# Performance work log

Hardware: AMD Instinct MI355X
Metric: run time of the kernel (lower is better)

## Reference

```python
import jax, jax.numpy as jnp
import numpy as np

B, N, L = 1, 256, 512
D_MSA, D_PAIR, H, D = 256, 128, 8, 32
SCALING = 1.0 / float(np.sqrt(D))
EPS = 1e-5


def layer_norm(x, g, b):
    mu = jnp.mean(x, axis=-1, keepdims=True)
    var = jnp.mean(jnp.square(x - mu), axis=-1, keepdims=True)
    return (x - mu) * jax.lax.rsqrt(var + EPS) * g + b


def setup_inputs() -> dict:
    key = jax.random.key(0)
    ks = jax.random.split(key, 16)
    inp = {
        "msa": jax.random.normal(ks[0], (B, N, L, D_MSA), dtype=jnp.float32),
        "pair": jax.random.normal(ks[1], (B, L, L, D_PAIR), dtype=jnp.float32),
        "ln_msa_g": 1.0 + 0.1 * jax.random.normal(ks[2], (D_MSA,), dtype=jnp.float32),
        "ln_msa_b": 0.1 * jax.random.normal(ks[3], (D_MSA,), dtype=jnp.float32),
        "ln_pair_g": 1.0 + 0.1 * jax.random.normal(ks[4], (D_PAIR,), dtype=jnp.float32),
        "ln_pair_b": 0.1 * jax.random.normal(ks[5], (D_PAIR,), dtype=jnp.float32),
        "w_q": 0.02 * jax.random.normal(ks[6], (D_MSA, H * D), dtype=jnp.float32),
        "w_k": 0.02 * jax.random.normal(ks[7], (D_MSA, H * D), dtype=jnp.float32),
        "w_v": 0.02 * jax.random.normal(ks[8], (D_MSA, H * D), dtype=jnp.float32),
        "w_b": 0.02 * jax.random.normal(ks[9], (D_PAIR, H), dtype=jnp.float32),
        "w_g": 0.02 * jax.random.normal(ks[10], (D_MSA, H * D), dtype=jnp.float32),
        "b_g": jnp.ones((H * D,), dtype=jnp.float32),
        "w_out": 0.02 * jax.random.normal(ks[11], (H * D, D_MSA), dtype=jnp.float32),
        "b_out": jnp.zeros((D_MSA,), dtype=jnp.float32),
        "mask": jax.random.randint(ks[12], (B, L), 0, 2, dtype=jnp.int32),
    }
    return inp


def reference(msa, pair, ln_msa_g, ln_msa_b, ln_pair_g, ln_pair_b,
              w_q, w_k, w_v, w_b, w_g, b_g, w_out, b_out, mask):
    # mask == 0 means padded/invalid position (torch: mask = mask == 0)
    pad = (mask == 0)  # [B, L] bool
    msa = jnp.nan_to_num(msa)
    pair = jnp.nan_to_num(pair)
    msa_n = layer_norm(msa, ln_msa_g, ln_msa_b)          # [B,N,L,d_msa]
    pair_n = layer_norm(pair, ln_pair_g, ln_pair_b)       # [B,L,L,d_pair]

    q = (msa_n @ w_q).reshape(B, N, L, H, D)
    k = (msa_n @ w_k).reshape(B, N, L, H, D)
    v = (msa_n @ w_v).reshape(B, N, L, H, D)
    bias = pair_n @ w_b                                    # [B,L,L,H]
    gate = jax.nn.sigmoid(msa_n @ w_g + b_g)               # [B,N,L,H*D]

    fill = pad[:, None, :, None, None]                     # [B,1,L,1,1]
    zero = jnp.zeros((), dtype=q.dtype)
    q = jnp.where(fill, zero, q)
    v = jnp.where(fill, zero, v)
    k = jnp.where(fill, zero, k) * jnp.asarray(SCALING, dtype=k.dtype)

    # reduce over both MSA-sequence dim n and head dim d
    attn = jnp.einsum('bnqhd,bnkhd->bqkh', q, k) + bias    # [B,L,L,H]
    mask2d = pad[:, :, None] | pad[:, None, :]             # [B,L,L]
    attn = jnp.where(mask2d[..., None], jnp.asarray(-1e9, attn.dtype), attn)
    attn = jax.nn.softmax(attn, axis=2)                    # softmax over k

    out = jnp.einsum('bqkh,bnkhd->bnqhd', attn, v).reshape(B, N, L, H * D)
    out = gate * out
    out = out @ w_out + b_out                              # [B,N,L,d_msa]
    out = jnp.where(pad[:, None, :, None], jnp.zeros((), out.dtype), out)
    return out
```

## Files before the change

kernel.cpp:

```cpp
#include <hip/hip_runtime.h>
#include <hip/hip_bf16.h>
#include <math.h>

typedef __bf16 bf16_t;
typedef float f32x4 __attribute__((ext_vector_type(4)));
typedef __bf16 bf16x8 __attribute__((ext_vector_type(8)));
typedef __bf16 bf16x4 __attribute__((ext_vector_type(4)));
typedef int i32x4 __attribute__((ext_vector_type(4)));

#define SCALING 0.17677669529663687f
#define LNEPS 1e-5f

#define OFF_QKG   0u
#define OFF_LOG   201326592u
#define OFF_BIAS  209715200u
#define OFF_P     218103808u
#define OFF_WT    222298112u
#define OFF_WTO   222822400u
#define OFF_FLAG  222953472u

#define GLOBAL_AS __attribute__((address_space(1)))
#define LDS_AS    __attribute__((address_space(3)))

static __device__ __forceinline__ f32x4 mfma16(bf16x8 a, bf16x8 b, f32x4 c) {
  return __builtin_amdgcn_mfma_f32_16x16x32_bf16(a, b, c, 0, 0, 0);
}

static __device__ __forceinline__ float ldf(const void* p, int i, int is32) {
  return is32 ? ((const float*)p)[i] : (float)((const bf16_t*)p)[i];
}
static __device__ __forceinline__ float scrubf(float x) {
  if (x != x) return 0.f;
  return fminf(fmaxf(x, -3.3e38f), 3.3e38f);
}

__global__ __launch_bounds__(256) void k_detect(const unsigned short* raw, int* flag) {
  __shared__ int s;
  int t = threadIdx.x;
  if (t == 0) s = 0;
  __syncthreads();
  int local = 0;
  for (int i = 0; i < 16; i++) {
    unsigned short u = raw[t * 16 + i];
    int e = (u >> 7) & 0xFF;
    if (e >= 170) local = 1;
  }
  if (local) s = 1;
  __syncthreads();
  if (t == 0) *flag = s;
}

__global__ __launch_bounds__(256) void k_transpose(
    const void* wq, const void* wk, const void* wv, const void* wg,
    const void* wout, const int* flag, bf16_t* wt_cat, bf16_t* wt_out) {
  int is32 = *flag;
  int idx = blockIdx.x * 256 + threadIdx.x;
  if (idx < 1024 * 256) {
    int c = idx >> 8, k = idx & 255;
    const void* src = (c < 256) ? wq : (c < 512) ? wk : (c < 768) ? wv : wg;
    wt_cat[c * 256 + (k ^ ((c & 7) << 3))] = (bf16_t)ldf(src, k * 256 + (c & 255), is32);
  } else {
    int i2 = idx - 1024 * 256;
    int c = i2 >> 8, k = i2 & 255;
    wt_out[c * 256 + k] = (bf16_t)ldf(wout, k * 256 + c, is32);
  }
}

__global__ __launch_bounds__(256) void k_ln(
    const void* msa, const void* g, const void* b, const int* flag,
    char* msaln, char* qkg_bytes) {
  int is32 = *flag;
  int t = threadIdx.x, lane = t & 63, w = t >> 6;
  int c0 = lane * 4;
  float gv[4], bv[4];
#pragma unroll
  for (int e = 0; e < 4; e++) { gv[e] = ldf(g, c0 + e, is32); bv[e] = ldf(b, c0 + e, is32); }
  int row0 = blockIdx.x * 64 + w * 16;
  for (int rr = 0; rr < 16; rr++) {
    int r = row0 + rr;
    float x[4];
    if (is32) {
      f32x4 v = *(const f32x4*)((const float*)msa + (size_t)r * 256 + c0);
#pragma unroll
      for (int e = 0; e < 4; e++) x[e] = scrubf(v[e]);
    } else {
      bf16x4 v = *(const bf16x4*)((const bf16_t*)msa + (size_t)r * 256 + c0);
#pragma unroll
      for (int e = 0; e < 4; e++) x[e] = scrubf((float)v[e]);
    }
    float s = x[0] + x[1] + x[2] + x[3];
    float sq = x[0] * x[0] + x[1] * x[1] + x[2] * x[2] + x[3] * x[3];
#pragma unroll
    for (int o = 32; o >= 1; o >>= 1) {
      s += __shfl_xor(s, o, 64);
      sq += __shfl_xor(sq, o, 64);
    }
    float mu = s * (1.f / 256.f);
    float var = sq * (1.f / 256.f) - mu * mu;
    float rs = rsqrtf(fmaxf(var, 0.f) + LNEPS);
    bf16x4 y;
#pragma unroll
    for (int e = 0; e < 4; e++) y[e] = (bf16_t)((x[e] - mu) * rs * gv[e] + bv[e]);
    int pc = (lane >> 1) ^ (r & 7);
    char* dst = is32 ? (msaln + (size_t)r * 512)
                     : (qkg_bytes + (size_t)r * 1536 + 512);
    *(bf16x4*)(dst + pc * 16 + (lane & 1) * 8) = y;
  }
}

__global__ __launch_bounds__(256) void k_pair_bias(
    const void* pair, const void* g, const void* b,
    const void* wb, const int* flag, float* bias_ws) {
  __shared__ float wbs[128 * 8];
  __shared__ float gs[128], bs[128];
  int is32 = *flag;
  int t = threadIdx.x;
  if (t < 128) { gs[t] = ldf(g, t, is32); bs[t] = ldf(b, t, is32); }
  for (int i = t; i < 1024; i += 256) wbs[i] = ldf(wb, i, is32);
  __syncthreads();
  int lane = t & 63, w = t >> 6;
  int j = lane & 7;
  int rowg = lane >> 3;
  float gr[16], br[16];
#pragma unroll
  for (int e = 0; e < 16; e++) { gr[e] = gs[j * 16 + e]; br[e] = bs[j * 16 + e]; }
  int row0 = blockIdx.x * 64 + w * 16;
#pragma unroll
  for (int pass = 0; pass < 2; pass++) {
    int row = row0 + pass * 8 + rowg;
    float x[16];
    if (is32) {
#pragma unroll
      for (int i = 0; i < 4; i++) {
        f32x4 v = *(const f32x4*)((const float*)pair + (size_t)row * 128 + j * 16 + i * 4);
#pragma unroll
        for (int e = 0; e < 4; e++) x[i * 4 + e] = scrubf(v[e]);
      }
    } else {
#pragma unroll
      for (int i = 0; i < 2; i++) {
        i32x4 raw = *(const i32x4*)((const bf16_t*)pair + (size_t)row * 128 + j * 16 + i * 8);
        const bf16_t* sp = (const bf16_t*)&raw;
#pragma unroll
        for (int e = 0; e < 8; e++) x[i * 8 + e] = scrubf((float)sp[e]);
      }
    }
    float s = 0.f, sq = 0.f;
#pragma unroll
    for (int e = 0; e < 16; e++) { s += x[e]; sq += x[e] * x[e]; }
#pragma unroll
    for (int o = 1; o <= 4; o <<= 1) {
      s += __shfl_xor(s, o, 64);
      sq += __shfl_xor(sq, o, 64);
    }
    float mu = s * (1.f / 128.f);
    float var = sq * (1.f / 128.f) - mu * mu;
    float rs = rsqrtf(fmaxf(var, 0.f) + LNEPS);
    float ph[8] = {0.f, 0.f, 0.f, 0.f, 0.f, 0.f, 0.f, 0.f};
#pragma unroll
    for (int e = 0; e < 16; e++) {
      float xn = (x[e] - mu) * rs * gr[e] + br[e];
      const float* wp = wbs + (j * 16 + e) * 8;
      f32x4 w0 = *(const f32x4*)wp;
      f32x4 w1 = *(const f32x4*)(wp + 4);
#pragma unroll
      for (int hh = 0; hh < 4; hh++) { ph[hh] += xn * w0[hh]; ph[4 + hh] += xn * w1[hh]; }
    }
#pragma unroll
    for (int o = 1; o <= 4; o <<= 1) {
#pragma unroll
      for (int hh = 0; hh < 8; hh++) ph[hh] += __shfl_xor(ph[hh], o, 64);
    }
    if (j == 0) {
      int qp = row >> 9, kp = row & 511;
      float* bp = bias_ws + (size_t)qp * 512 + kp;
#pragma unroll
      for (int hh = 0; hh < 8; hh++) bp[(size_t)hh * 262144] = ph[hh];
    }
  }
}

static __device__ __forceinline__ void issue_b(const bf16_t* wtc, int col0, int half,
                                               char* dst, int t) {
#pragma unroll
  for (int j = 0; j < 8; ++j) {
    int o = t * 16 + j * 4096;
    int row = o >> 8, within = o & 255;
    const char* src = (const char*)wtc + (size_t)(col0 + row) * 512 + half * 256 + within;
    __builtin_amdgcn_global_load_lds((const GLOBAL_AS void*)src,
                                     (LDS_AS void*)(dst + o), 16, 0, 0);
  }
}

__global__ __launch_bounds__(256, 2) void k_proj(
    const bf16_t* wt_cat, const void* bg, const int* mask, const int* flag,
    const char* msaln, bf16_t* qkg, bf16_t* vt) {
  __shared__ __align__(16) char lds[65536];
  char* B0 = lds + 32768;
  char* B1 = lds;
  int is32 = *flag;
  int t = threadIdx.x, lane = t & 63, wc = t >> 6;
  int hi = lane >> 4, cl = lane & 15;
  int row0 = blockIdx.x * 64;
  int rbase = row0 + hi * 4;

  unsigned padbits = 0;
#pragma unroll
  for (int m = 0; m < 4; ++m)
#pragma unroll
    for (int i = 0; i < 4; ++i)
      if (mask[(rbase + m * 16 + i) & 511] == 0) padbits |= 1u << (m * 4 + i);
  float bgv[2][2];
#pragma unroll
  for (int bb = 0; bb < 2; ++bb)
#pragma unroll
    for (int n = 0; n < 2; ++n)
      bgv[bb][n] = ldf(bg, bb * 128 + wc * 32 + n * 16 + cl, is32);

  {
    const char* abase = is32 ? msaln : ((const char*)qkg + 512);
    size_t astride = is32 ? 512 : 1536;
#pragma unroll
    for (int j = 0; j < 8; ++j) {
      int o = t * 16 + j * 4096;
      int row = o >> 9, within = o & 511;
      const char* src = abase + (size_t)(row0 + row) * astride + within;
      __builtin_amdgcn_global_load_lds((const GLOBAL_AS void*)src,
                                       (LDS_AS void*)(lds + o), 16, 0, 0);
    }
  }
  issue_b(wt_cat, 0, 0, B0, t);
  __syncthreads();

  bf16x8 aall[8][4];
#pragma unroll
  for (int ks = 0; ks < 8; ++ks)
#pragma unroll
    for (int m = 0; m < 4; ++m)
      aall[ks][m] = *(const bf16x8*)(lds + (size_t)(cl + m * 16) * 512 +
                                     (((ks * 4 + hi) ^ (cl & 7)) << 4));
  __syncthreads();

  int brow0 = wc * 32 + cl, brow1 = brow0 + 16;
  int sb = (cl & 7) << 4;
  f32x4 z = {0.f, 0.f, 0.f, 0.f};
  f32x4 acc[4][2] = {{z, z}, {z, z}, {z, z}, {z, z}};

  for (int bn = 0; bn < 8; ++bn) {
    issue_b(wt_cat, bn << 7, 1, B1, t);
#pragma unroll
    for (int kk = 0; kk < 4; ++kk) {
      int k8 = (kk * 4 + hi) << 4;
      bf16x8 b0 = *(const bf16x8*)(B0 + brow0 * 256 + (k8 ^ sb));
      bf16x8 b1 = *(const bf16x8*)(B0 + brow1 * 256 + (k8 ^ sb));
#pragma unroll
      for (int m = 0; m < 4; ++m) {
        acc[m][0] = mfma16(aall[kk][m], b0, acc[m][0]);
        acc[m][1] = mfma16(aall[kk][m], b1, acc[m][1]);
      }
    }
    __syncthreads();
    if (bn < 7) issue_b(wt_cat, (bn + 1) << 7, 0, B0, t);
#pragma unroll
    for (int kk = 0; kk < 4; ++kk) {
      int k8 = (kk * 4 + hi) << 4;
      bf16x8 b0 = *(const bf16x8*)(B1 + brow0 * 256 + (k8 ^ sb));
      bf16x8 b1 = *(const bf16x8*)(B1 + brow1 * 256 + (k8 ^ sb));
#pragma unroll
      for (int m = 0; m < 4; ++m) {
        acc[m][0] = mfma16(aall[4 + kk][m], b0, acc[m][0]);
        acc[m][1] = mfma16(aall[4 + kk][m], b1, acc[m][1]);
      }
    }
    __syncthreads();
    int region = bn >> 1, col0 = bn << 7;
    if (region == 2) {
#pragma unroll
      for (int m = 0; m < 4; ++m) {
#pragma unroll
        for (int n = 0; n < 2; ++n) {
          int col = col0 + wc * 32 + n * 16 + cl;
          int hd = col & 255;
          int rb = rbase + m * 16;
          bf16x4 y;
#pragma unroll
          for (int i = 0; i < 4; ++i)
            y[i] = (bf16_t)(((padbits >> (m * 4 + i)) & 1) ? 0.f : acc[m][n][i]);
          *(bf16x4*)(vt + ((size_t)((rb >> 9) * 8 + (hd >> 5)) * 32 + (hd & 31)) * 512 +
                     (rb & 511)) = y;
          acc[m][n] = z;
        }
      }
    } else {
#pragma unroll
      for (int m = 0; m < 4; ++m) {
#pragma unroll
        for (int n = 0; n < 2; ++n) {
          int col = col0 + wc * 32 + n * 16 + cl;
#pragma unroll
          for (int i = 0; i < 4; ++i) {
            int r = rbase + m * 16 + i;
            bool pad = (padbits >> (m * 4 + i)) & 1;
            float v = acc[m][n][i];
            if (region == 0) {
              qkg[(size_t)r * 768 + col] = (bf16_t)(pad ? 0.f : v);
            } else if (region == 1) {
              qkg[(size_t)r * 768 + col] = (bf16_t)(pad ? 0.f : v * SCALING);
            } else {
              float xg = v + bgv[bn & 1][n];
              qkg[(size_t)r * 768 + 512 + (col & 255)] = (bf16_t)(1.f / (1.f + __expf(-xg)));
            }
          }
          acc[m][n] = z;
        }
      }
    }
  }
}

__global__ __launch_bounds__(256) void k_logits(const bf16_t* qkg, float* logit_ws) {
  __shared__ bf16_t As[64 * 136];
  __shared__ bf16_t Bs[64 * 136];
  int t = threadIdx.x, lane = t & 63, w = t >> 6;
  int j = blockIdx.x;
  int jj = (j & 7) * 64 + (j >> 3);
  int ktile = jj & 7, qtile = (jj >> 3) & 7, h = jj >> 6;
  int mw = w & 1, nw = w >> 1;
  f32x4 z = {0.f, 0.f, 0.f, 0.f};
  f32x4 acc[2][2] = {{z, z}, {z, z}};
  for (int s = 0; s < 64; s++) {
    int kk0 = s * 128;
#pragma unroll
    for (int i = 0; i < 4; i++) {
      int flat = t + i * 256;
      int r = flat >> 4, c8 = flat & 15;
      int kk = kk0 + c8 * 8;
      int n = kk >> 5, d = kk & 31;
      i32x4 va = *(const i32x4*)(qkg + ((size_t)(n * 512 + qtile * 64 + r)) * 768 + h * 32 + d);
      *(i32x4*)(As + r * 136 + c8 * 8) = va;
      i32x4 vb = *(const i32x4*)(qkg + ((size_t)(n * 512 + ktile * 64 + r)) * 768 + 256 + h * 32 + d);
      *(i32x4*)(Bs + r * 136 + c8 * 8) = vb;
    }
    __syncthreads();
#pragma unroll
    for (int kk = 0; kk < 128; kk += 32) {
      int ko = kk + (lane >> 4) * 8;
      bf16x8 a0 = *(const bf16x8*)(As + (mw * 32 + (lane & 15)) * 136 + ko);
      bf16x8 a1 = *(const bf16x8*)(As + (mw * 32 + 16 + (lane & 15)) * 136 + ko);
      bf16x8 b0 = *(const bf16x8*)(Bs + (nw * 32 + (lane & 15)) * 136 + ko);
      bf16x8 b1 = *(const bf16x8*)(Bs + (nw * 32 + 16 + (lane & 15)) * 136 + ko);
      acc[0][0] = mfma16(a0, b0, acc[0][0]);
      acc[0][1] = mfma16(a0, b1, acc[0][1]);
      acc[1][0] = mfma16(a1, b0, acc[1][0]);
      acc[1][1] = mfma16(a1, b1, acc[1][1]);
    }
    __syncthreads();
  }
  int quad = lane >> 4, cl = lane & 15;
#pragma unroll
  for (int mt = 0; mt < 2; mt++) {
#pragma unroll
    for (int nt = 0; nt < 2; nt++) {
      int kp = ktile * 64 + nw * 32 + nt * 16 + cl;
#pragma unroll
      for (int i = 0; i < 4; i++) {
        int q = qtile * 64 + mw * 32 + mt * 16 + quad * 4 + i;
        logit_ws[((size_t)(h * 512 + q)) * 512 + kp] = acc[mt][nt][i];
      }
    }
  }
}

__global__ __launch_bounds__(256) void k_softmax(
    const float* logit_ws, const float* bias_ws, const int* mask, bf16_t* p_ws) {
  __shared__ float red[8];
  int t = threadIdx.x;
  int hq = blockIdx.x;
  int q = hq & 511;
  bool padq = (mask[q] == 0);
  const float* lg = logit_ws + (size_t)hq * 512;
  const float* bi = bias_ws + (size_t)(hq >> 9) * 262144 + (size_t)q * 512;
  int k0 = t * 2;
  float v0 = lg[k0] + bi[k0];
  float v1 = lg[k0 + 1] + bi[k0 + 1];
  if (padq || mask[k0] == 0) v0 = -1e9f;
  if (padq || mask[k0 + 1] == 0) v1 = -1e9f;
  float m = fmaxf(v0, v1);
#pragma unroll
  for (int o = 32; o >= 1; o >>= 1) m = fmaxf(m, __shfl_xor(m, o, 64));
  if ((t & 63) == 0) red[t >> 6] = m;
  __syncthreads();
  m = fmaxf(fmaxf(red[0], red[1]), fmaxf(red[2], red[3]));
  float e0 = __expf(v0 - m), e1 = __expf(v1 - m);
  float s = e0 + e1;
#pragma unroll
  for (int o = 32; o >= 1; o >>= 1) s += __shfl_xor(s, o, 64);
  if ((t & 63) == 0) red[4 + (t >> 6)] = s;
  __syncthreads();
  s = red[4] + red[5] + red[6] + red[7];
  float inv = 1.f / s;
  p_ws[(size_t)hq * 512 + k0] = (bf16_t)(e0 * inv);
  p_ws[(size_t)hq * 512 + k0 + 1] = (bf16_t)(e1 * inv);
}

__global__ __launch_bounds__(256) void k_av(
    const bf16_t* p_ws, const bf16_t* vt, bf16_t* qkg) {
  __shared__ bf16_t Ps[64 * 136];
  __shared__ bf16_t Vs[32 * 136];
  int t = threadIdx.x, lane = t & 63, w = t >> 6;
  int j = blockIdx.x;
  int jj = (j & 7) * 2048 + (j >> 3);
  int qt = jj & 7;
  int n = (jj >> 3) & 255;
  int h = jj >> 11;
  f32x4 z = {0.f, 0.f, 0.f, 0.f};
  f32x4 acc[2] = {z, z};
  for (int s = 0; s < 4; s++) {
    int k0 = s * 128;
#pragma unroll
    for (int i = 0; i < 4; i++) {
      int flat = t + i * 256;
      int r = flat >> 4, c8 = flat & 15;
      *(i32x4*)(Ps + r * 136 + c8 * 8) =
          *(const i32x4*)(p_ws + ((size_t)(h * 512 + qt * 64 + r)) * 512 + k0 + c8 * 8);
    }
#pragma unroll
    for (int i = 0; i < 2; i++) {
      int flat = t + i * 256;
      int r = flat >> 4, c8 = flat & 15;
      *(i32x4*)(Vs + r * 136 + c8 * 8) =
          *(const i32x4*)(vt + ((size_t)((n * 8 + h) * 32 + r)) * 512 + k0 + c8 * 8);
    }
    __syncthreads();
#pragma unroll
    for (int kk = 0; kk < 128; kk += 32) {
      int ko = kk + (lane >> 4) * 8;
      bf16x8 a = *(const bf16x8*)(Ps + (w * 16 + (lane & 15)) * 136 + ko);
      bf16x8 b0 = *(const bf16x8*)(Vs + ((lane & 15)) * 136 + ko);
      bf16x8 b1 = *(const bf16x8*)(Vs + (16 + (lane & 15)) * 136 + ko);
      acc[0] = mfma16(a, b0, acc[0]);
      acc[1] = mfma16(a, b1, acc[1]);
    }
    __syncthreads();
  }
  int quad = lane >> 4, cl = lane & 15;
#pragma unroll
  for (int nt = 0; nt < 2; nt++) {
#pragma unroll
    for (int i = 0; i < 4; i++) {
      int q = qt * 64 + w * 16 + quad * 4 + i;
      int d = nt * 16 + cl;
      size_t base = ((size_t)(n * 512 + q)) * 768;
      float gate = (float)qkg[base + 512 + h * 32 + d];
      qkg[base + h * 32 + d] = (bf16_t)(acc[nt][i] * gate);
    }
  }
}

__global__ __launch_bounds__(256) void k_out(
    const bf16_t* qkg, const bf16_t* wt_out, const void* b_out,
    const int* mask, const int* flag, void* outp) {
  __shared__ bf16_t As[64 * 72];
  __shared__ bf16_t Bs[256 * 72];
  int is32 = *flag;
  int t = threadIdx.x, lane = t & 63, w = t >> 6;
  int row0 = blockIdx.x * 64;
  int hi = lane >> 4, cl = lane & 15;
  f32x4 z = {0.f, 0.f, 0.f, 0.f};
  f32x4 acc[4][4];
#pragma unroll
  for (int m = 0; m < 4; ++m)
#pragma unroll
    for (int n = 0; n < 4; ++n) acc[m][n] = z;
  for (int kt = 0; kt < 4; kt++) {
#pragma unroll
    for (int i = 0; i < 2; i++) {
      int flat = t + i * 256;
      int r = flat >> 3, c8 = flat & 7;
      *(i32x4*)(As + r * 72 + c8 * 8) =
          *(const i32x4*)(qkg + (size_t)(row0 + r) * 768 + kt * 64 + c8 * 8);
    }
#pragma unroll
    for (int i = 0; i < 8; i++) {
      int flat = t + i * 256;
      int r = flat >> 3, c8 = flat & 7;
      *(i32x4*)(Bs + r * 72 + c8 * 8) =
          *(const i32x4*)(wt_out + (size_t)r * 256 + kt * 64 + c8 * 8);
    }
    __syncthreads();
#pragma unroll
    for (int kk = 0; kk < 64; kk += 32) {
      int ko = kk + hi * 8;
      bf16x8 a[4], b[4];
#pragma unroll
      for (int m = 0; m < 4; ++m)
        a[m] = *(const bf16x8*)(As + (m * 16 + cl) * 72 + ko);
#pragma unroll
      for (int n = 0; n < 4; ++n)
        b[n] = *(const bf16x8*)(Bs + (w * 64 + n * 16 + cl) * 72 + ko);
#pragma unroll
      for (int m = 0; m < 4; ++m)
#pragma unroll
        for (int n = 0; n < 4; ++n) acc[m][n] = mfma16(a[m], b[n], acc[m][n]);
    }
    __syncthreads();
  }
#pragma unroll
  for (int n = 0; n < 4; ++n) {
    int col = w * 64 + n * 16 + cl;
    float bo = ldf(b_out, col, is32);
#pragma unroll
    for (int m = 0; m < 4; ++m) {
#pragma unroll
      for (int i = 0; i < 4; ++i) {
        int r = row0 + m * 16 + hi * 4 + i;
        int l = r & 511;
        float v = acc[m][n][i] + bo;
        if (mask[l] == 0) v = 0.f;
        if (is32) ((float*)outp)[(size_t)r * 256 + col] = v;
        else ((bf16_t*)outp)[(size_t)r * 256 + col] = (bf16_t)v;
      }
    }
  }
}

extern "C" void kernel_launch(void* const* d_in, const int* in_sizes, int n_in,
                              void* d_out, int out_size, void* d_ws, size_t ws_size,
                              hipStream_t stream) {
  const void* msa      = d_in[0];
  const void* pair     = d_in[1];
  const void* ln_msa_g = d_in[2];
  const void* ln_msa_b = d_in[3];
  const void* ln_pair_g= d_in[4];
  const void* ln_pair_b= d_in[5];
  const void* w_q      = d_in[6];
  const void* w_k      = d_in[7];
  const void* w_v      = d_in[8];
  const void* w_b      = d_in[9];
  const void* w_g      = d_in[10];
  const void* b_g      = d_in[11];
  const void* w_out    = d_in[12];
  const void* b_out    = d_in[13];
  const int*  mask     = (const int*)d_in[14];

  char* ws = (char*)d_ws;
  bf16_t* qkg   = (bf16_t*)(ws + OFF_QKG);
  float*  logit = (float*)(ws + OFF_LOG);
  float*  biasb = (float*)(ws + OFF_BIAS);
  bf16_t* pbuf  = (bf16_t*)(ws + OFF_P);
  bf16_t* wtc   = (bf16_t*)(ws + OFF_WT);
  bf16_t* wto   = (bf16_t*)(ws + OFF_WTO);
  int*    flag  = (int*)(ws + OFF_FLAG);
  bf16_t* vt    = (bf16_t*)d_out;
  char*   msaln = (char*)d_out + 67108864u;

  k_detect<<<1, 256, 0, stream>>>((const unsigned short*)msa, flag);
  k_transpose<<<1280, 256, 0, stream>>>(w_q, w_k, w_v, w_g, w_out, flag, wtc, wto);
  k_ln<<<2048, 256, 0, stream>>>(msa, ln_msa_g, ln_msa_b, flag, msaln, (char*)qkg);
  k_pair_bias<<<4096, 256, 0, stream>>>(pair, ln_pair_g, ln_pair_b, w_b, flag, biasb);
  k_proj<<<2048, 256, 0, stream>>>(wtc, b_g, mask, flag, msaln, qkg, vt);
  k_logits<<<512, 256, 0, stream>>>(qkg, logit);
  k_softmax<<<4096, 256, 0, stream>>>(logit, biasb, mask, pbuf);
  k_av<<<16384, 256, 0, stream>>>(pbuf, vt, qkg);
  k_out<<<2048, 256, 0, stream>>>(qkg, wto, b_out, mask, flag, d_out);
}
```

Baseline: 790.8 us.

## Restructure logits and AV kernels with async LDS loads, swizzling and register-resident P

k_logits now uses 128x128 tiles with 512 threads, split-K over two halves of the MSA dimension. Operands are double-buffered through global_load_lds with an XOR-swizzled LDS layout. The second K-half accumulates directly into the bias buffer, which removes a separate add. k_av keeps a 128-row P tile in registers and streams 16 sequences of V through double-buffered LDS, so P is no longer reloaded for each sequence. V and P are written in swizzled layouts to match, which ties the producer and consumer kernels to the same layout and raises register pressure in k_av.

After: 752.3 us. 1.05x faster.

```diff
diff --git a/kernel.cpp b/kernel.cpp
--- a/kernel.cpp
+++ b/kernel.cpp
@@ -281,13 +281,16 @@
         for (int n = 0; n < 2; ++n) {
           int col = col0 + wc * 32 + n * 16 + cl;
           int hd = col & 255;
+          int d = hd & 31;
           int rb = rbase + m * 16;
+          int l = rb & 511;
           bf16x4 y;
 #pragma unroll
           for (int i = 0; i < 4; ++i)
             y[i] = (bf16_t)(((padbits >> (m * 4 + i)) & 1) ? 0.f : acc[m][n][i]);
-          *(bf16x4*)(vt + ((size_t)((rb >> 9) * 8 + (hd >> 5)) * 32 + (hd & 31)) * 512 +
-                     (rb & 511)) = y;
+          *(bf16x4*)((char*)vt +
+                     ((size_t)((rb >> 9) * 8 + (hd >> 5)) * 32 + d) * 1024 +
+                     (((l >> 3) ^ (d & 7)) << 4) + ((l & 7) << 1)) = y;
           acc[m][n] = z;
         }
       }
@@ -318,54 +321,78 @@
   }
 }
 
-__global__ __launch_bounds__(256) void k_logits(const bf16_t* qkg, float* logit_ws) {
-  __shared__ bf16_t As[64 * 136];
-  __shared__ bf16_t Bs[64 * 136];
+__global__ __launch_bounds__(512) void k_logits(
+    const bf16_t* qkg, float* logit_ws, float* bias_ws) {
+  __shared__ __align__(16) char lds[131072];
   int t = threadIdx.x, lane = t & 63, w = t >> 6;
   int j = blockIdx.x;
-  int jj = (j & 7) * 64 + (j >> 3);
-  int ktile = jj & 7, qtile = (jj >> 3) & 7, h = jj >> 6;
-  int mw = w & 1, nw = w >> 1;
+  int h = j & 7, rest = j >> 3;
+  int kt = rest & 3, qt = (rest >> 2) & 3, ks = rest >> 4;
+  int qw = w >> 2, kw = w & 3;
+  int hi = lane >> 4, cl = lane & 15;
+  int q0 = qt * 128, k0 = kt * 128;
+
+  auto issue = [&](int step, char* buf) {
+    int n0 = ks * 128 + step * 4;
+#pragma unroll
+    for (int jj = 0; jj < 4; ++jj) {
+      int o = t * 16 + jj * 8192;
+      int r = o >> 8, p = (o & 255) >> 4;
+      int l = p ^ (r & 7);
+      const char* src = (const char*)qkg +
+          ((size_t)(n0 + (l >> 2)) * 512 + q0 + r) * 1536 + h * 64 + (l & 3) * 16;
+      __builtin_amdgcn_global_load_lds((const GLOBAL_AS void*)src,
+                                       (LDS_AS void*)(buf + o), 16, 0, 0);
+    }
+#pragma unroll
+    for (int jj = 0; jj < 4; ++jj) {
+      int o = t * 16 + jj * 8192;
+      int r = o >> 8, p = (o & 255) >> 4;
+      int l = p ^ (r & 7);
+      const char* src = (const char*)qkg +
+          ((size_t)(n0 + (l >> 2)) * 512 + k0 + r) * 1536 + 512 + h * 64 + (l & 3) * 16;
+      __builtin_amdgcn_global_load_lds((const GLOBAL_AS void*)src,
+                                       (LDS_AS void*)(buf + 32768 + o), 16, 0, 0);
+    }
+  };
+
   f32x4 z = {0.f, 0.f, 0.f, 0.f};
-  f32x4 acc[2][2] = {{z, z}, {z, z}};
-  for (int s = 0; s < 64; s++) {
-    int kk0 = s * 128;
-#pragma unroll
-    for (int i = 0; i < 4; i++) {
-      int flat = t + i * 256;
-      int r = flat >> 4, c8 = flat & 15;
-      int kk = kk0 + c8 * 8;
-      int n = kk >> 5, d = kk & 31;
-      i32x4 va = *(const i32x4*)(qkg + ((size_t)(n * 512 + qtile * 64 + r)) * 768 + h * 32 + d);
-      *(i32x4*)(As + r * 136 + c8 * 8) = va;
-      i32x4 vb = *(const i32x4*)(qkg + ((size_t)(n * 512 + ktile * 64 + r)) * 768 + 256 + h * 32 + d);
-      *(i32x4*)(Bs + r * 136 + c8 * 8) = vb;
+  f32x4 acc[4][2] = {{z, z}, {z, z}, {z, z}, {z, z}};
+  issue(0, lds);
+  __syncthreads();
+  for (int step = 0; step < 32; ++step) {
+    char* buf = lds + (step & 1) * 65536;
+    if (step < 31) issue(step + 1, lds + ((step + 1) & 1) * 65536);
+    char* Ab = buf;
+    char* Bb = buf + 32768;
+#pragma unroll
+    for (int ku = 0; ku < 4; ++ku) {
+      int ch = ((ku * 4 + hi) ^ (cl & 7)) << 4;
+      bf16x8 a[4], b[2];
+#pragma unroll
+      for (int m = 0; m < 4; ++m)
+        a[m] = *(const bf16x8*)(Ab + (qw * 64 + m * 16 + cl) * 256 + ch);
+#pragma unroll
+      for (int n = 0; n < 2; ++n)
+        b[n] = *(const bf16x8*)(Bb + (kw * 32 + n * 16 + cl) * 256 + ch);
+#pragma unroll
+      for (int m = 0; m < 4; ++m)
+#pragma unroll
+        for (int n = 0; n < 2; ++n) acc[m][n] = mfma16(a[m], b[n], acc[m][n]);
     }
     __syncthreads();
-#pragma unroll
-    for (int kk = 0; kk < 128; kk += 32) {
-      int ko = kk + (lane >> 4) * 8;
-      bf16x8 a0 = *(const bf16x8*)(As + (mw * 32 + (lane & 15)) * 136 + ko);
-      bf16x8 a1 = *(const bf16x8*)(As + (mw * 32 + 16 + (lane & 15)) * 136 + ko);
-      bf16x8 b0 = *(const bf16x8*)(Bs + (nw * 32 + (lane & 15)) * 136 + ko);
-      bf16x8 b1 = *(const bf16x8*)(Bs + (nw * 32 + 16 + (lane & 15)) * 136 + ko);
-      acc[0][0] = mfma16(a0, b0, acc[0][0]);
-      acc[0][1] = mfma16(a0, b1, acc[0][1]);
-      acc[1][0] = mfma16(a1, b0, acc[1][0]);
-      acc[1][1] = mfma16(a1, b1, acc[1][1]);
-    }
-    __syncthreads();
-  }
-  int quad = lane >> 4, cl = lane & 15;
-#pragma unroll
-  for (int mt = 0; mt < 2; mt++) {
-#pragma unroll
-    for (int nt = 0; nt < 2; nt++) {
-      int kp = ktile * 64 + nw * 32 + nt * 16 + cl;
-#pragma unroll
-      for (int i = 0; i < 4; i++) {
-        int q = qtile * 64 + mw * 32 + mt * 16 + quad * 4 + i;
-        logit_ws[((size_t)(h * 512 + q)) * 512 + kp] = acc[mt][nt][i];
+  }
+#pragma unroll
+  for (int m = 0; m < 4; ++m) {
+#pragma unroll
+    for (int n = 0; n < 2; ++n) {
+      int k = k0 + kw * 32 + n * 16 + cl;
+#pragma unroll
+      for (int i = 0; i < 4; ++i) {
+        int q = q0 + qw * 64 + m * 16 + hi * 4 + i;
+        size_t idx = ((size_t)(h * 512 + q)) * 512 + k;
+        if (ks == 0) logit_ws[idx] = acc[m][n][i];
+        else bias_ws[idx] += acc[m][n][i];
       }
     }
   }
@@ -399,61 +426,90 @@
   __syncthreads();
   s = red[4] + red[5] + red[6] + red[7];
   float inv = 1.f / s;
-  p_ws[(size_t)hq * 512 + k0] = (bf16_t)(e0 * inv);
-  p_ws[(size_t)hq * 512 + k0 + 1] = (bf16_t)(e1 * inv);
-}
-
-__global__ __launch_bounds__(256) void k_av(
+  int chunk = (t >> 2) ^ (q & 7);
+  bf16_t* pp = (bf16_t*)((char*)p_ws + (size_t)hq * 1024 + chunk * 16 + (t & 3) * 4);
+  pp[0] = (bf16_t)(e0 * inv);
+  pp[1] = (bf16_t)(e1 * inv);
+}
+
+__global__ __launch_bounds__(512, 2) void k_av(
     const bf16_t* p_ws, const bf16_t* vt, bf16_t* qkg) {
-  __shared__ bf16_t Ps[64 * 136];
-  __shared__ bf16_t Vs[32 * 136];
+  __shared__ __align__(16) char lds[65536];
   int t = threadIdx.x, lane = t & 63, w = t >> 6;
+  int hi = lane >> 4, cl = lane & 15;
   int j = blockIdx.x;
-  int jj = (j & 7) * 2048 + (j >> 3);
-  int qt = jj & 7;
-  int n = (jj >> 3) & 255;
-  int h = jj >> 11;
+  int h = j & 7, rest = j >> 3;
+  int ng = rest >> 2, qt = rest & 3;
+  int q0 = qt * 128;
+
+  const char* pbase = (const char*)p_ws + ((size_t)h * 512 + q0) * 1024;
+  bf16x8 pf[16];
+#pragma unroll
+  for (int jj = 0; jj < 8; ++jj) {
+    int o = t * 16 + jj * 8192;
+    __builtin_amdgcn_global_load_lds((const GLOBAL_AS void*)(pbase + o),
+                                     (LDS_AS void*)(lds + o), 16, 0, 0);
+  }
+  __syncthreads();
+  if (w < 4) {
+    int lr = w * 16 + cl;
+#pragma unroll
+    for (int ks = 0; ks < 16; ++ks)
+      pf[ks] = *(const bf16x8*)(lds + lr * 1024 + (((ks * 4 + hi) ^ (cl & 7)) << 4));
+  }
+  __syncthreads();
+#pragma unroll
+  for (int jj = 0; jj < 8; ++jj) {
+    int o = t * 16 + jj * 8192;
+    __builtin_amdgcn_global_load_lds((const GLOBAL_AS void*)(pbase + 65536 + o),
+                                     (LDS_AS void*)(lds + o), 16, 0, 0);
+  }
+  __syncthreads();
+  if (w >= 4) {
+    int lr = (w - 4) * 16 + cl;
+#pragma unroll
+    for (int ks = 0; ks < 16; ++ks)
+      pf[ks] = *(const bf16x8*)(lds + lr * 1024 + (((ks * 4 + hi) ^ (cl & 7)) << 4));
+  }
+  __syncthreads();
+
+  char* V0 = lds;
+  char* V1 = lds + 32768;
+  auto issue_v = [&](int nn, char* dst) {
+    const char* src = (const char*)vt + ((size_t)((ng * 16 + nn) * 8 + h) * 32) * 1024;
+#pragma unroll
+    for (int jj = 0; jj < 4; ++jj) {
+      int o = t * 16 + jj * 8192;
+      __builtin_amdgcn_global_load_lds((const GLOBAL_AS void*)(src + o),
+                                       (LDS_AS void*)(dst + o), 16, 0, 0);
+    }
+  };
+  issue_v(0, V0);
+  __syncthreads();
+  int Lb = q0 + w * 16 + hi * 4;
   f32x4 z = {0.f, 0.f, 0.f, 0.f};
-  f32x4 acc[2] = {z, z};
-  for (int s = 0; s < 4; s++) {
-    int k0 = s * 128;
-#pragma unroll
-    for (int i = 0; i < 4; i++) {
-      int flat = t + i * 256;
-      int r = flat >> 4, c8 = flat & 15;
-      *(i32x4*)(Ps + r * 136 + c8 * 8) =
-          *(const i32x4*)(p_ws + ((size_t)(h * 512 + qt * 64 + r)) * 512 + k0 + c8 * 8);
-    }
-#pragma unroll
-    for (int i = 0; i < 2; i++) {
-      int flat = t + i * 256;
-      int r = flat >> 4, c8 = flat & 15;
-      *(i32x4*)(Vs + r * 136 + c8 * 8) =
-          *(const i32x4*)(vt + ((size_t)((n * 8 + h) * 32 + r)) * 512 + k0 + c8 * 8);
+  for (int nn = 0; nn < 16; ++nn) {
+    char* cur = (nn & 1) ? V1 : V0;
+    if (nn < 15) issue_v(nn + 1, (nn & 1) ? V0 : V1);
+    f32x4 a0 = z, a1 = z;
+#pragma unroll
+    for (int ks = 0; ks < 16; ++ks) {
+      int ch = ((ks * 4 + hi) ^ (cl & 7)) << 4;
+      bf16x8 b0 = *(const bf16x8*)(cur + cl * 1024 + ch);
+      bf16x8 b1 = *(const bf16x8*)(cur + (16 + cl) * 1024 + ch);
+      a0 = mfma16(pf[ks], b0, a0);
+      a1 = mfma16(pf[ks], b1, a1);
+    }
+    int n = ng * 16 + nn;
+#pragma unroll
+    for (int i = 0; i < 4; ++i) {
+      size_t base = ((size_t)n * 512 + Lb + i) * 768 + h * 32 + cl;
+      float g0 = (float)qkg[base + 512];
+      float g1 = (float)qkg[base + 512 + 16];
+      qkg[base] = (bf16_t)(a0[i] * g0);
+      qkg[base + 16] = (bf16_t)(a1[i] * g1);
     }
     __syncthreads();
-#pragma unroll
-    for (int kk = 0; kk < 128; kk += 32) {
-      int ko = kk + (lane >> 4) * 8;
-      bf16x8 a = *(const bf16x8*)(Ps + (w * 16 + (lane & 15)) * 136 + ko);
-      bf16x8 b0 = *(const bf16x8*)(Vs + ((lane & 15)) * 136 + ko);
-      bf16x8 b1 = *(const bf16x8*)(Vs + (16 + (lane & 15)) * 136 + ko);
-      acc[0] = mfma16(a, b0, acc[0]);
-      acc[1] = mfma16(a, b1, acc[1]);
-    }
-    __syncthreads();
-  }
-  int quad = lane >> 4, cl = lane & 15;
-#pragma unroll
-  for (int nt = 0; nt < 2; nt++) {
-#pragma unroll
-    for (int i = 0; i < 4; i++) {
-      int q = qt * 64 + w * 16 + quad * 4 + i;
-      int d = nt * 16 + cl;
-      size_t base = ((size_t)(n * 512 + q)) * 768;
-      float gate = (float)qkg[base + 512 + h * 32 + d];
-      qkg[base + h * 32 + d] = (bf16_t)(acc[nt][i] * gate);
-    }
   }
 }
 
@@ -559,8 +615,8 @@
   k_ln<<<2048, 256, 0, stream>>>(msa, ln_msa_g, ln_msa_b, flag, msaln, (char*)qkg);
   k_pair_bias<<<4096, 256, 0, stream>>>(pair, ln_pair_g, ln_pair_b, w_b, flag, biasb);
   k_proj<<<2048, 256, 0, stream>>>(wtc, b_g, mask, flag, msaln, qkg, vt);
-  k_logits<<<512, 256, 0, stream>>>(qkg, logit);
+  k_logits<<<256, 512, 0, stream>>>(qkg, logit, biasb);
   k_softmax<<<4096, 256, 0, stream>>>(logit, biasb, mask, pbuf);
-  k_av<<<16384, 256, 0, stream>>>(pbuf, vt, qkg);
+  k_av<<<512, 512, 0, stream>>>(pbuf, vt, qkg);
   k_out<<<2048, 256, 0, stream>>>(qkg, wto, b_out, mask, flag, d_out);
 }
```
